# Kernel tuning notes

Hardware: AMD Instinct MI355X
Metric: run time of the kernel (lower is better)

## Reference

```python
import jax, jax.numpy as jnp
import numpy as np

N, E, H, FN, FE = 50000, 800000, 128, 8, 4


def setup_inputs() -> dict:
    key = jax.random.key(0)
    ks = jax.random.split(key, 12)
    g = lambda k, shape: jax.random.normal(k, shape, dtype=jnp.float32) * 0.05
    return dict(
        x=jax.random.normal(ks[0], (N, FN), dtype=jnp.float32),
        edge_index=jax.random.randint(ks[1], (2, E), 0, N),
        edge_attr=jax.random.normal(ks[2], (E, FE), dtype=jnp.float32),
        W1=g(ks[3], (FN, H)), b1=jnp.zeros((H,), jnp.float32),
        W2=g(ks[4], (H, H)), b2=jnp.zeros((H,), jnp.float32),
        W3=g(ks[5], (H, H)), b3=jnp.zeros((H,), jnp.float32),
        We1=g(ks[6], (FE, H)), be1=jnp.zeros((H,), jnp.float32),
        We2=g(ks[7], (H, H)), be2=jnp.zeros((H,), jnp.float32),
        Wc1=g(ks[8], (3 * H, H)), bc1=jnp.zeros((H,), jnp.float32),
        Wc2=g(ks[9], (H, H // 2)), bc2=jnp.zeros((H // 2,), jnp.float32),
        Wc3=g(ks[10], (H // 2, 2)), bc3=jnp.zeros((2,), jnp.float32),
    )


def _gcn(h, W, b, row2, col2, norm, n):
    # GCNConv: transform, normalized message from source row2 -> target col2, scatter-add, bias
    h = h @ W
    msg = norm[:, None] * h[row2]  # [E+N, H]
    return jax.ops.segment_sum(msg, col2, num_segments=n) + b


def reference(x, edge_index, edge_attr, W1, b1, W2, b2, W3, b3,
              We1, be1, We2, be2, Wc1, bc1, Wc2, bc2, Wc3, bc3):
    n = x.shape[0]
    row, col = edge_index[0], edge_index[1]
    loop = jnp.arange(n)
    # add self-loops (PyG GCNConv default)
    row2 = jnp.concatenate([row, loop])
    col2 = jnp.concatenate([col, loop])
    deg = jax.ops.segment_sum(jnp.ones_like(col2, dtype=x.dtype), col2, num_segments=n)
    dinv = jnp.where(deg > 0, deg ** -0.5, 0.0)
    norm = dinv[row2] * dinv[col2]  # symmetric normalization per edge

    h = jax.nn.relu(_gcn(x, W1, b1, row2, col2, norm, n))
    h = jax.nn.relu(_gcn(h, W2, b2, row2, col2, norm, n))
    h = jax.nn.relu(_gcn(h, W3, b3, row2, col2, norm, n))

    # edge encoder MLP (dropout inactive in eval)
    ef = jax.nn.relu(edge_attr @ We1 + be1) @ We2 + be2

    # gather endpoint node features, concat with edge features
    ec = jnp.concatenate([h[row], h[col], ef], axis=1)  # [E, 3H]
    z = jax.nn.relu(ec @ Wc1 + bc1)
    z = jax.nn.relu(z @ Wc2 + bc2)
    logits = z @ Wc3 + bc3
    return jax.nn.log_softmax(logits, axis=1)
```

## Files before the change

kernel.cpp:

```cpp
#include <hip/hip_runtime.h>
#include <math.h>

#define H 128
#define STC 152
#define SOT 136
#define SPQ 136
#define Z2S 69

typedef __attribute__((ext_vector_type(8))) short short8;
typedef __attribute__((ext_vector_type(4))) float f32x4;

__device__ inline unsigned short f2bf(float f) {
    unsigned int u = __float_as_uint(f);
    return (unsigned short)((u + 0x7fffu + ((u >> 16) & 1u)) >> 16);
}
__device__ inline float bflo(unsigned int v) { return __uint_as_float(v << 16); }
__device__ inline float bfhi(unsigned int v) { return __uint_as_float(v & 0xffff0000u); }
__device__ inline float bf2f(unsigned short v) { return __uint_as_float(((unsigned int)v) << 16); }

__device__ inline void fma4(float4& acc, float a, const float4 w) {
    acc.x = fmaf(a, w.x, acc.x);
    acc.y = fmaf(a, w.y, acc.y);
    acc.z = fmaf(a, w.z, acc.z);
    acc.w = fmaf(a, w.w, acc.w);
}


__global__ void count_kernel(const int* __restrict__ col, int E, int* __restrict__ cnt) {
    int e = blockIdx.x * blockDim.x + threadIdx.x;
    if (e < E) atomicAdd(&cnt[col[e]], 1);
}

__global__ void scan_sum_kernel(const int* __restrict__ cnt, int N, int* __restrict__ bsum) {
    int b = blockIdx.x, t = threadIdx.x;
    int base = b * 1024 + t * 4;
    int s = 0;
#pragma unroll
    for (int g = 0; g < 4; ++g) {
        int i = base + g;
        if (i < N) s += cnt[i];
    }
    for (int off = 32; off >= 1; off >>= 1) s += __shfl_down(s, off, 64);
    __shared__ int ws[4];
    if ((t & 63) == 0) ws[t >> 6] = s;
    __syncthreads();
    if (t == 0) bsum[b] = ws[0] + ws[1] + ws[2] + ws[3];
}

__global__ void scan_offsets_kernel(const int* __restrict__ bsum, int nb,
                                    int* __restrict__ boff, int* __restrict__ col_start, int N) {
    int lane = threadIdx.x;
    int v = (lane < nb) ? bsum[lane] : 0;
    int incl = v;
    for (int off = 1; off < 64; off <<= 1) {
        int u = __shfl_up(incl, off, 64);
        if (lane >= off) incl += u;
    }
    if (lane < nb) boff[lane] = incl - v;
    if (lane == 63) col_start[N] = incl;
}

__global__ void scan_write_kernel(const int* __restrict__ cnt, int N, const int* __restrict__ boff,
                                  int* __restrict__ col_start, int* __restrict__ cursor,
                                  float* __restrict__ dinv) {
    int b = blockIdx.x, t = threadIdx.x;
    int lane = t & 63, wv = t >> 6;
    int base = b * 1024 + t * 4;
    int c[4];
    int s = 0;
#pragma unroll
    for (int g = 0; g < 4; ++g) {
        int i = base + g;
        c[g] = (i < N) ? cnt[i] : 0;
        s += c[g];
    }
    int incl = s;
    for (int off = 1; off < 64; off <<= 1) {
        int u = __shfl_up(incl, off, 64);
        if (lane >= off) incl += u;
    }
    __shared__ int ws[4];
    if (lane == 63) ws[wv] = incl;
    __syncthreads();
    int run = boff[b] + incl - s;
    for (int w = 0; w < wv; ++w) run += ws[w];
#pragma unroll
    for (int g = 0; g < 4; ++g) {
        int i = base + g;
        if (i < N) {
            col_start[i] = run;
            cursor[i] = run;
            dinv[i] = rsqrtf((float)(c[g] + 1));
            run += c[g];
        }
    }
}

__global__ void scatter_kernel(const int* __restrict__ row, const int* __restrict__ col, int E,
                               int* __restrict__ cursor, int* __restrict__ csc_src,
                               int2* __restrict__ csc_ec) {
    int e = blockIdx.x * blockDim.x + threadIdx.x;
    if (e < E) {
        int c = col[e];
        int p = atomicAdd(&cursor[c], 1);
        csc_src[p] = row[e];
        csc_ec[p] = make_int2(e, c);
    }
}


__global__ __launch_bounds__(256) void aggx_kernel(
    const float* __restrict__ x, const int* __restrict__ col_start,
    const int* __restrict__ csc_src, const float* __restrict__ dinv,
    float* __restrict__ aggx, int N) {
    int wv = threadIdx.x >> 6, lane = threadIdx.x & 63;
    int i = blockIdx.x * 4 + wv;
    if (i >= N) return;
    int f = lane & 7, j = lane >> 3;
    int s0 = col_start[i], s1 = col_start[i + 1];
    float acc = 0.f;
    int p = s0 + j;
    for (; p + 8 < s1; p += 16) {
        int sa = csc_src[p], sb = csc_src[p + 8];
        float va = dinv[sa] * x[sa * 8 + f];
        float vb = dinv[sb] * x[sb * 8 + f];
        acc += va + vb;
    }
    if (p < s1) {
        int s = csc_src[p];
        acc = fmaf(dinv[s], x[s * 8 + f], acc);
    }
    acc += __shfl_xor(acc, 8, 64);
    acc += __shfl_xor(acc, 16, 64);
    acc += __shfl_xor(acc, 32, 64);
    if (j == 0) {
        float di = dinv[i];
        aggx[i * 8 + f] = fmaf(di, acc, di * di * x[i * 8 + f]);
    }
}

__global__ void xform8bf_kernel(const float* __restrict__ aggx, const float* __restrict__ W,
                                const float* __restrict__ b, const float* __restrict__ dinv,
                                unsigned int* __restrict__ out, int N) {
    int t = blockIdx.x * 256 + threadIdx.x;
    int i = t >> 6, jp = t & 63;
    if (i >= N) return;
    const float* ar = aggx + i * 8;
    float sc = dinv[i];
    int j0 = jp * 2;
    float a0 = b[j0], a1 = b[j0 + 1];
#pragma unroll
    for (int k = 0; k < 8; ++k) {
        float av = ar[k];
        a0 = fmaf(av, W[k * 128 + j0], a0);
        a1 = fmaf(av, W[k * 128 + j0 + 1], a1);
    }
    out[(size_t)i * 64 + jp] = (unsigned int)f2bf(sc * fmaxf(a0, 0.f)) |
                               ((unsigned int)f2bf(sc * fmaxf(a1, 0.f)) << 16);
}

__global__ __launch_bounds__(256) void agg128bf_kernel(
    const unsigned int* __restrict__ hd, const int* __restrict__ col_start,
    const int* __restrict__ csc_src, const float* __restrict__ dinv,
    unsigned int* __restrict__ out, int N) {
    int wv = threadIdx.x >> 6, lane = threadIdx.x & 63;
    int i = blockIdx.x * 4 + wv;
    if (i >= N) return;
    int s0 = col_start[i], s1 = col_start[i + 1];
    float ax = 0.f, ay = 0.f;
    int p = s0;
    for (; p + 16 <= s1; p += 16) {
        unsigned int v[16];
#pragma unroll
        for (int k = 0; k < 16; ++k)
            v[k] = hd[(size_t)csc_src[p + k] * 64 + lane];
#pragma unroll
        for (int k = 0; k < 16; ++k) { ax += bflo(v[k]); ay += bfhi(v[k]); }
    }
    for (; p + 4 <= s1; p += 4) {
        unsigned int v0 = hd[(size_t)csc_src[p + 0] * 64 + lane];
        unsigned int v1 = hd[(size_t)csc_src[p + 1] * 64 + lane];
        unsigned int v2 = hd[(size_t)csc_src[p + 2] * 64 + lane];
        unsigned int v3 = hd[(size_t)csc_src[p + 3] * 64 + lane];
        ax += bflo(v0) + bflo(v1) + bflo(v2) + bflo(v3);
        ay += bfhi(v0) + bfhi(v1) + bfhi(v2) + bfhi(v3);
    }
    for (; p < s1; ++p) {
        unsigned int v = hd[(size_t)csc_src[p] * 64 + lane];
        ax += bflo(v); ay += bfhi(v);
    }
    float di = dinv[i];
    unsigned int vs = hd[(size_t)i * 64 + lane];
    float rx = di * (ax + bflo(vs));
    float ry = di * (ay + bfhi(vs));
    out[(size_t)i * 64 + lane] = (unsigned int)f2bf(rx) | ((unsigned int)f2bf(ry) << 16);
}

__global__ __launch_bounds__(256) void xform_mfma_kernel(
    const unsigned short* __restrict__ in, const unsigned short* __restrict__ Bp,
    const float* __restrict__ b, const float* __restrict__ scale,
    unsigned short* __restrict__ out, int N) {
    __shared__ __align__(16) unsigned short sm[64 * STC];
    int tid = threadIdx.x;
    int i0 = blockIdx.x * 64;
    for (int u = tid; u < 1024; u += 256) {
        int i = u >> 4, l = u & 15;
        int node = i0 + i; if (node >= N) node = N - 1;
        uint4 v = ((const uint4*)in)[(size_t)node * 16 + l];
        *(uint4*)&sm[i * STC + l * 8] = v;
    }
    __syncthreads();
    int lane = tid & 63, w = tid >> 6, lm = lane & 15, quad = lane >> 4;
    int nt0 = 2 * w, nt1 = 2 * w + 1;
    f32x4 acc0[4], acc1[4];
    {
        float bv0 = b[nt0 * 16 + lm], bv1 = b[nt1 * 16 + lm];
        for (int m = 0; m < 4; ++m)
            for (int r = 0; r < 4; ++r) { acc0[m][r] = bv0; acc1[m][r] = bv1; }
    }
#pragma unroll
    for (int s = 0; s < 4; ++s) {
        short8 b0 = *(const short8*)&Bp[((size_t)(s * 8 + nt0) * 64 + lane) * 8];
        short8 b1 = *(const short8*)&Bp[((size_t)(s * 8 + nt1) * 64 + lane) * 8];
#pragma unroll
        for (int m = 0; m < 4; ++m) {
            short8 afr = *(const short8*)&sm[(m * 16 + lm) * STC + s * 32 + quad * 8];
            acc0[m] = __builtin_amdgcn_mfma_f32_16x16x32_bf16(afr, b0, acc0[m], 0, 0, 0);
            acc1[m] = __builtin_amdgcn_mfma_f32_16x16x32_bf16(afr, b1, acc1[m], 0, 0, 0);
        }
    }
    __syncthreads();
    for (int m = 0; m < 4; ++m)
        for (int r = 0; r < 4; ++r) {
            int rw = m * 16 + quad * 4 + r;
            int node = i0 + rw; if (node >= N) node = N - 1;
            float sc = scale ? scale[node] : 1.f;
            sm[rw * SOT + nt0 * 16 + lm] = f2bf(sc * fmaxf(acc0[m][r], 0.f));
            sm[rw * SOT + nt1 * 16 + lm] = f2bf(sc * fmaxf(acc1[m][r], 0.f));
        }
    __syncthreads();
    for (int u = tid; u < 1024; u += 256) {
        int i = u >> 4, l = u & 15;
        int node = i0 + i;
        if (node < N)
            *(uint4*)&out[(size_t)node * 128 + l * 8] = *(uint4*)&sm[i * SOT + l * 8];
    }
}


__global__ void weff_kernel(const float* __restrict__ We2, const float* __restrict__ Wc1,
                            float* __restrict__ Weff) {
    int idx = blockIdx.x * blockDim.x + threadIdx.x;
    int k = idx >> 7, c = idx & 127;
    float acc = 0.f;
    for (int j = 0; j < 128; ++j)
        acc = fmaf(We2[k * 128 + j], Wc1[(256 + j) * 128 + c], acc);
    Weff[idx] = acc;
}

__global__ void bc1p_kernel(const float* __restrict__ bc1, const float* __restrict__ be2,
                            const float* __restrict__ Wc1, float* __restrict__ bc1p) {
    int c = threadIdx.x;
    float acc = bc1[c];
    for (int j = 0; j < 128; ++j)
        acc = fmaf(be2[j], Wc1[(256 + j) * 128 + c], acc);
    bc1p[c] = acc;
}

__global__ void packg_kernel(const float* __restrict__ src, unsigned short* __restrict__ dst) {
    int idx = blockIdx.x * 256 + threadIdx.x;
    int s = idx >> 9, nt = (idx >> 6) & 7, lane = idx & 63;
    int quad = lane >> 4, lm = lane & 15;
    int n = nt * 16 + lm, k0 = s * 32 + quad * 8;
    unsigned int p[4];
#pragma unroll
    for (int g = 0; g < 4; ++g) {
        p[g] = (unsigned int)f2bf(src[(k0 + 2 * g) * 128 + n]) |
               ((unsigned int)f2bf(src[(k0 + 2 * g + 1) * 128 + n]) << 16);
    }
    *(uint4*)&dst[(size_t)idx * 8] = make_uint4(p[0], p[1], p[2], p[3]);
}

__global__ void pack2_kernel(const float* __restrict__ Wc2, unsigned short* __restrict__ Bp2) {
    int idx = blockIdx.x * 256 + threadIdx.x;
    int s = idx >> 8, nt = (idx >> 6) & 3, lane = idx & 63;
    int quad = lane >> 4, lm = lane & 15;
    int n = nt * 16 + lm, k0 = s * 32 + quad * 8;
    unsigned int p[4];
#pragma unroll
    for (int g = 0; g < 4; ++g) {
        p[g] = (unsigned int)f2bf(Wc2[(k0 + 2 * g) * 64 + n]) |
               ((unsigned int)f2bf(Wc2[(k0 + 2 * g + 1) * 64 + n]) << 16);
    }
    *(uint4*)&Bp2[(size_t)idx * 8] = make_uint4(p[0], p[1], p[2], p[3]);
}

__global__ void packwe1_kernel(const float* __restrict__ We1, const float* __restrict__ be1,
                               unsigned short* __restrict__ BpE) {
    int idx = blockIdx.x * 256 + threadIdx.x;
    if (idx >= 512) return;
    int nt = idx >> 6, lane = idx & 63;
    int quad = lane >> 4, lm = lane & 15;
    int n = nt * 16 + lm, k0 = quad * 8;
    unsigned int p[4];
#pragma unroll
    for (int g = 0; g < 4; ++g) {
        int r0 = k0 + 2 * g, r1 = r0 + 1;
        float v0 = (r0 < 4) ? We1[r0 * 128 + n] : ((r0 == 4) ? be1[n] : 0.f);
        float v1 = (r1 < 4) ? We1[r1 * 128 + n] : ((r1 == 4) ? be1[n] : 0.f);
        p[g] = (unsigned int)f2bf(v0) | ((unsigned int)f2bf(v1) << 16);
    }
    *(uint4*)&BpE[(size_t)idx * 8] = make_uint4(p[0], p[1], p[2], p[3]);
}


__global__ __launch_bounds__(256) void h3pq_kernel(
    const unsigned short* __restrict__ in, const unsigned short* __restrict__ BpW3,
    const float* __restrict__ b3,
    const unsigned short* __restrict__ BpA, const unsigned short* __restrict__ BpB,
    const float* __restrict__ bc1p,
    unsigned short* __restrict__ P, unsigned short* __restrict__ Q, int N) {
    __shared__ __align__(16) unsigned short At[64 * STC];
    __shared__ __align__(16) unsigned short Hs[64 * SOT];
    int tid = threadIdx.x;
    int i0 = blockIdx.x * 64;
    for (int u = tid; u < 1024; u += 256) {
        int i = u >> 4, l = u & 15;
        int node = i0 + i; if (node >= N) node = N - 1;
        uint4 v = ((const uint4*)in)[(size_t)node * 16 + l];
        *(uint4*)&At[i * STC + l * 8] = v;
    }
    __syncthreads();
    int lane = tid & 63, w = tid >> 6, lm = lane & 15, quad = lane >> 4;

    {
        int nt0 = 2 * w, nt1 = 2 * w + 1;
        f32x4 a0[4], a1[4];
        float bv0 = b3[nt0 * 16 + lm], bv1 = b3[nt1 * 16 + lm];
        for (int m = 0; m < 4; ++m)
            for (int r = 0; r < 4; ++r) { a0[m][r] = bv0; a1[m][r] = bv1; }
#pragma unroll
        for (int s = 0; s < 4; ++s) {
            short8 b0 = *(const short8*)&BpW3[((size_t)(s * 8 + nt0) * 64 + lane) * 8];
            short8 b1 = *(const short8*)&BpW3[((size_t)(s * 8 + nt1) * 64 + lane) * 8];
#pragma unroll
            for (int m = 0; m < 4; ++m) {
                short8 afr = *(const short8*)&At[(m * 16 + lm) * STC + s * 32 + quad * 8];
                a0[m] = __builtin_amdgcn_mfma_f32_16x16x32_bf16(afr, b0, a0[m], 0, 0, 0);
                a1[m] = __builtin_amdgcn_mfma_f32_16x16x32_bf16(afr, b1, a1[m], 0, 0, 0);
            }
        }
        __syncthreads();
        for (int m = 0; m < 4; ++m)
            for (int r = 0; r < 4; ++r) {
                int rw = m * 16 + quad * 4 + r;
                Hs[rw * SOT + nt0 * 16 + lm] = f2bf(fmaxf(a0[m][r], 0.f));
                Hs[rw * SOT + nt1 * 16 + lm] = f2bf(fmaxf(a1[m][r], 0.f));
            }
    }
    __syncthreads();

    int half = w & 1;
    const unsigned short* Bp = (w >> 1) ? BpB : BpA;
    f32x4 acc[4][4];
    for (int nt = 0; nt < 4; ++nt) {
        float bv = (w >> 1) ? 0.f : bc1p[half * 64 + nt * 16 + lm];
        for (int m = 0; m < 4; ++m)
            for (int r = 0; r < 4; ++r) acc[nt][m][r] = bv;
    }
#pragma unroll
    for (int s = 0; s < 4; ++s) {
        short8 afr[4];
#pragma unroll
        for (int m = 0; m < 4; ++m)
            afr[m] = *(const short8*)&Hs[(m * 16 + lm) * SOT + s * 32 + quad * 8];
#pragma unroll
        for (int nt = 0; nt < 4; ++nt) {
            short8 bfr = *(const short8*)&Bp[((size_t)(s * 8 + half * 4 + nt) * 64 + lane) * 8];
#pragma unroll
            for (int m = 0; m < 4; ++m)
                acc[nt][m] = __builtin_amdgcn_mfma_f32_16x16x32_bf16(afr[m], bfr, acc[nt][m], 0, 0, 0);
        }
    }
    __syncthreads();
    unsigned short* St = At;

    if (w < 2) {
        for (int nt = 0; nt < 4; ++nt)
            for (int m = 0; m < 4; ++m)
                for (int r = 0; r < 4; ++r) {
                    int rw = m * 16 + quad * 4 + r;
                    St[rw * SOT + half * 64 + nt * 16 + lm] = f2bf(acc[nt][m][r]);
                }
    }
    __syncthreads();
    for (int u = tid; u < 1024; u += 256) {
        int i = u >> 4, l = u & 15;
        int node = i0 + i;
        if (node < N)
            *(uint4*)&P[(size_t)node * 128 + l * 8] = *(uint4*)&St[i * SOT + l * 8];
    }
    __syncthreads();
    if (w >= 2) {
        for (int nt = 0; nt < 4; ++nt)
            for (int m = 0; m < 4; ++m)
                for (int r = 0; r < 4; ++r) {
                    int rw = m * 16 + quad * 4 + r;
                    St[rw * SOT + half * 64 + nt * 16 + lm] = f2bf(acc[nt][m][r]);
                }
    }
    __syncthreads();
    for (int u = tid; u < 1024; u += 256) {
        int i = u >> 4, l = u & 15;
        int node = i0 + i;
        if (node < N)
            *(uint4*)&Q[(size_t)node * 128 + l * 8] = *(uint4*)&St[i * SOT + l * 8];
    }
}


__global__ __launch_bounds__(256, 4) void classifier_mfma2(
    const int* __restrict__ csc_src, const int2* __restrict__ csc_ec,
    const float* __restrict__ ea, const unsigned short* __restrict__ BpE,
    const unsigned short* __restrict__ P, const unsigned short* __restrict__ Q,
    const unsigned short* __restrict__ BpU, const unsigned short* __restrict__ Bp2,
    const float* __restrict__ bc2, const float* __restrict__ Wc3, const float* __restrict__ bc3,
    float* __restrict__ out, int E) {
    __shared__ __align__(16) unsigned char smem[37888];
    unsigned short* SpqB = (unsigned short*)smem;
    float* z2 = (float*)smem;
    unsigned short* At = (unsigned short*)(smem + 17664);
    unsigned short* z1 = At;
    float* part = (float*)(smem + 17664);
    int* sS = (int*)(smem + 37120);
    int* eS = sS + 64;
    int* cS = eS + 64;

    int tid = threadIdx.x;
    int lane = tid & 63, w = tid >> 6, lm = lane & 15, quad = lane >> 4;
    int e0 = blockIdx.x * 64;

    short8 bE0 = *(const short8*)&BpE[((size_t)(2 * w) * 64 + lane) * 8];
    short8 bE1 = *(const short8*)&BpE[((size_t)(2 * w + 1) * 64 + lane) * 8];
    short8 b0s[4], b1s[4], b2s[4];
#pragma unroll
    for (int s = 0; s < 4; ++s) {
        b0s[s] = *(const short8*)&BpU[((size_t)(s * 8 + 2 * w) * 64 + lane) * 8];
        b1s[s] = *(const short8*)&BpU[((size_t)(s * 8 + 2 * w + 1) * 64 + lane) * 8];
        b2s[s] = *(const short8*)&Bp2[((size_t)(s * 4 + w) * 64 + lane) * 8];
    }
    float bv2 = bc2[w * 16 + lm];

    if (tid < 64) {
        int p = e0 + tid; if (p >= E) p = E - 1;
        sS[tid] = csc_src[p];
        int2 ec = csc_ec[p];
        eS[tid] = ec.x; cS[tid] = ec.y;
    }
    __syncthreads();

    {
        const uint4* P4 = (const uint4*)P;
        const uint4* Q4 = (const uint4*)Q;
        int l = tid & 15;
#pragma unroll
        for (int j = 0; j < 4; ++j) {
            int i = (tid >> 4) + 16 * j;
            uint4 pv = P4[(size_t)sS[i] * 16 + l];
            uint4 qv = Q4[(size_t)cS[i] * 16 + l];
            unsigned int o0 = (unsigned int)f2bf(bflo(pv.x) + bflo(qv.x)) |
                              ((unsigned int)f2bf(bfhi(pv.x) + bfhi(qv.x)) << 16);
            unsigned int o1 = (unsigned int)f2bf(bflo(pv.y) + bflo(qv.y)) |
                              ((unsigned int)f2bf(bfhi(pv.y) + bfhi(qv.y)) << 16);
            unsigned int o2 = (unsigned int)f2bf(bflo(pv.z) + bflo(qv.z)) |
                              ((unsigned int)f2bf(bfhi(pv.z) + bfhi(qv.z)) << 16);
            unsigned int o3 = (unsigned int)f2bf(bflo(pv.w) + bflo(qv.w)) |
                              ((unsigned int)f2bf(bfhi(pv.w) + bfhi(qv.w)) << 16);
            *(uint4*)&SpqB[i * SPQ + l * 8] = make_uint4(o0, o1, o2, o3);
        }
    }

    short8 eaf[4];
#pragma unroll
    for (int m = 0; m < 4; ++m) eaf[m] = (short8){0, 0, 0, 0, 0, 0, 0, 0};
    if (quad == 0) {
#pragma unroll
        for (int m = 0; m < 4; ++m) {
            int ed = eS[m * 16 + lm];
            float4 a = ((const float4*)ea)[ed];
            eaf[m][0] = (short)f2bf(a.x);
            eaf[m][1] = (short)f2bf(a.y);
            eaf[m][2] = (short)f2bf(a.z);
            eaf[m][3] = (short)f2bf(a.w);
            eaf[m][4] = (short)0x3F80;
        }
    }

    {
        f32x4 zacc = {0.f, 0.f, 0.f, 0.f};
#pragma unroll
        for (int m = 0; m < 4; ++m) {
            f32x4 t0 = __builtin_amdgcn_mfma_f32_16x16x32_bf16(eaf[m], bE0, zacc, 0, 0, 0);
            f32x4 t1 = __builtin_amdgcn_mfma_f32_16x16x32_bf16(eaf[m], bE1, zacc, 0, 0, 0);
#pragma unroll
            for (int r = 0; r < 4; ++r) {
                int rw = m * 16 + quad * 4 + r;
                At[rw * STC + 32 * w + lm]      = f2bf(fmaxf(t0[r], 0.f));
                At[rw * STC + 32 * w + 16 + lm] = f2bf(fmaxf(t1[r], 0.f));
            }
        }
    }
    __syncthreads();

    f32x4 acc0[4], acc1[4];
    for (int m = 0; m < 4; ++m)
        for (int r = 0; r < 4; ++r) { acc0[m][r] = 0.f; acc1[m][r] = 0.f; }
#pragma unroll
    for (int s = 0; s < 4; ++s) {
#pragma unroll
        for (int m = 0; m < 4; ++m) {
            short8 afr = *(const short8*)&At[(m * 16 + lm) * STC + s * 32 + quad * 8];
            acc0[m] = __builtin_amdgcn_mfma_f32_16x16x32_bf16(afr, b0s[s], acc0[m], 0, 0, 0);
            acc1[m] = __builtin_amdgcn_mfma_f32_16x16x32_bf16(afr, b1s[s], acc1[m], 0, 0, 0);
        }
    }
    for (int m = 0; m < 4; ++m)
        for (int r = 0; r < 4; ++r) {
            int rw = m * 16 + quad * 4 + r;
            acc0[m][r] = fmaxf(acc0[m][r] + bf2f(SpqB[rw * SPQ + 32 * w + lm]), 0.f);
            acc1[m][r] = fmaxf(acc1[m][r] + bf2f(SpqB[rw * SPQ + 32 * w + 16 + lm]), 0.f);
        }
    __syncthreads();
    for (int m = 0; m < 4; ++m)
        for (int r = 0; r < 4; ++r) {
            int rw = m * 16 + quad * 4 + r;
            z1[rw * STC + 32 * w + lm]      = f2bf(acc0[m][r]);
            z1[rw * STC + 32 * w + 16 + lm] = f2bf(acc1[m][r]);
        }
    __syncthreads();

    {
        f32x4 acc2[4];
        for (int m = 0; m < 4; ++m)
            for (int r = 0; r < 4; ++r) acc2[m][r] = bv2;
#pragma unroll
        for (int s = 0; s < 4; ++s) {
#pragma unroll
            for (int m = 0; m < 4; ++m) {
                short8 afr = *(const short8*)&z1[(m * 16 + lm) * STC + s * 32 + quad * 8];
                acc2[m] = __builtin_amdgcn_mfma_f32_16x16x32_bf16(afr, b2s[s], acc2[m], 0, 0, 0);
            }
        }
        for (int m = 0; m < 4; ++m)
            for (int r = 0; r < 4; ++r)
                z2[(m * 16 + quad * 4 + r) * Z2S + w * 16 + lm] = fmaxf(acc2[m][r], 0.f);
    }
    __syncthreads();

    {
        int e = tid & 63, q = tid >> 6;
        int c = q & 1, hf = q >> 1;
        const float* zr = z2 + e * Z2S + hf * 32;
        const float* wc = Wc3 + hf * 64 + c;
        float acc = 0.f;
#pragma unroll 8
        for (int kk = 0; kk < 32; ++kk)
            acc = fmaf(zr[kk], wc[2 * kk], acc);
        part[q * 64 + e] = acc;
    }
    __syncthreads();
    if (tid < 64) {
        int p = e0 + tid;
        if (p < E) {
            float l0 = bc3[0] + part[tid] + part[128 + tid];
            float l1 = bc3[1] + part[64 + tid] + part[192 + tid];
            float m = fmaxf(l0, l1);
            float lse = m + logf(expf(l0 - m) + expf(l1 - m));
            ((float2*)out)[eS[tid]] = make_float2(l0 - lse, l1 - lse);
        }
    }
}


extern "C" void kernel_launch(void* const* d_in, const int* in_sizes, int n_in,
                              void* d_out, int out_size, void* d_ws, size_t ws_size,
                              hipStream_t stream) {
    const float* x   = (const float*)d_in[0];
    const int*   ei  = (const int*)d_in[1];
    const float* ea  = (const float*)d_in[2];
    const float* W1  = (const float*)d_in[3];
    const float* b1  = (const float*)d_in[4];
    const float* W2  = (const float*)d_in[5];
    const float* b2  = (const float*)d_in[6];
    const float* W3  = (const float*)d_in[7];
    const float* b3  = (const float*)d_in[8];
    const float* We1 = (const float*)d_in[9];
    const float* be1 = (const float*)d_in[10];
    const float* We2 = (const float*)d_in[11];
    const float* be2 = (const float*)d_in[12];
    const float* Wc1 = (const float*)d_in[13];
    const float* bc1 = (const float*)d_in[14];
    const float* Wc2 = (const float*)d_in[15];
    const float* bc2 = (const float*)d_in[16];
    const float* Wc3 = (const float*)d_in[17];
    const float* bc3 = (const float*)d_in[18];
    float* out = (float*)d_out;

    int N = in_sizes[0] / 8;
    int E = in_sizes[1] / 2;
    const int* row = ei;
    const int* col = ei + E;
    int NB = (N + 1023) / 1024;
    int ntiles = (E + 63) / 64;

    char* w = (char*)d_ws;
    auto alloc = [&](size_t bytes) { void* p = (void*)w; w += (bytes + 255) & ~(size_t)255; return p; };
    int*   cnt       = (int*)alloc((size_t)N * 4);
    int*   col_start = (int*)alloc((size_t)(N + 1) * 4);
    int*   cursor    = (int*)alloc((size_t)N * 4);
    int*   csc_src   = (int*)alloc((size_t)E * 4);
    int2*  csc_ec    = (int2*)alloc((size_t)E * 8);
    float* dinv      = (float*)alloc((size_t)N * 4);
    int*   bsum      = (int*)alloc(64 * 4);
    int*   boff      = (int*)alloc(64 * 4);
    float* Weff      = (float*)alloc(128 * 128 * 4);
    float* bc1p      = (float*)alloc(128 * 4);
    unsigned short* BpA  = (unsigned short*)alloc(32768);
    unsigned short* BpB  = (unsigned short*)alloc(32768);
    unsigned short* BpU  = (unsigned short*)alloc(32768);
    unsigned short* BpW2 = (unsigned short*)alloc(32768);
    unsigned short* BpW3 = (unsigned short*)alloc(32768);
    unsigned short* Bp2  = (unsigned short*)alloc(16384);
    unsigned short* BpE  = (unsigned short*)alloc(8192);
    float* aggx = (float*)alloc((size_t)N * 8 * 4);
    unsigned short* bufA = (unsigned short*)alloc((size_t)N * H * 2);
    unsigned short* bufB = (unsigned short*)alloc((size_t)N * H * 2);
    unsigned short* Pm   = (unsigned short*)alloc((size_t)N * H * 2);
    unsigned short* Qm   = (unsigned short*)alloc((size_t)N * H * 2);

    hipMemsetAsync(cnt, 0, (size_t)N * 4, stream);
    count_kernel<<<(E + 255) / 256, 256, 0, stream>>>(col, E, cnt);
    scan_sum_kernel<<<NB, 256, 0, stream>>>(cnt, N, bsum);
    scan_offsets_kernel<<<1, 64, 0, stream>>>(bsum, NB, boff, col_start, N);
    scan_write_kernel<<<NB, 256, 0, stream>>>(cnt, N, boff, col_start, cursor, dinv);
    scatter_kernel<<<(E + 255) / 256, 256, 0, stream>>>(row, col, E, cursor, csc_src, csc_ec);

    weff_kernel<<<64, 256, 0, stream>>>(We2, Wc1, Weff);
    bc1p_kernel<<<1, 128, 0, stream>>>(bc1, be2, Wc1, bc1p);
    packg_kernel<<<8, 256, 0, stream>>>(Wc1, BpA);
    packg_kernel<<<8, 256, 0, stream>>>(Wc1 + 128 * 128, BpB);
    packg_kernel<<<8, 256, 0, stream>>>(Weff, BpU);
    packg_kernel<<<8, 256, 0, stream>>>(W2, BpW2);
    packg_kernel<<<8, 256, 0, stream>>>(W3, BpW3);
    pack2_kernel<<<4, 256, 0, stream>>>(Wc2, Bp2);
    packwe1_kernel<<<2, 256, 0, stream>>>(We1, be1, BpE);

    aggx_kernel<<<(N + 3) / 4, 256, 0, stream>>>(x, col_start, csc_src, dinv, aggx, N);
    xform8bf_kernel<<<(N * 64 + 255) / 256, 256, 0, stream>>>(aggx, W1, b1, dinv,
                                                              (unsigned int*)bufA, N);
    agg128bf_kernel<<<(N + 3) / 4, 256, 0, stream>>>((const unsigned int*)bufA, col_start, csc_src,
                                                     dinv, (unsigned int*)bufB, N);
    xform_mfma_kernel<<<(N + 63) / 64, 256, 0, stream>>>(bufB, BpW2, b2, dinv, bufA, N);
    agg128bf_kernel<<<(N + 3) / 4, 256, 0, stream>>>((const unsigned int*)bufA, col_start, csc_src,
                                                     dinv, (unsigned int*)bufB, N);
    h3pq_kernel<<<(N + 63) / 64, 256, 0, stream>>>(bufB, BpW3, b3, BpA, BpB, bc1p, Pm, Qm, N);

    classifier_mfma2<<<ntiles, 256, 0, stream>>>(
        csc_src, csc_ec, ea, BpE, Pm, Qm, BpU, Bp2, bc2, Wc3, bc3, out, E);
}
```

Baseline: 461.7 us.

## Process four edge tiles per classifier block with P-row prefetch and hardware bf16 packing

The classifier kernel now handles four 64-edge tiles per block. It loads all edge indices at once and prefetches the next tile's P rows into registers while the current tile's MFMA work runs, amortizing per-block weight-fragment loads and hiding gather latency. Separately, the software round-to-nearest float-to-bf16 conversion is replaced everywhere with the v_cvt_pk_bf16_f32 instruction, which packs two values per op. The cost is fewer blocks (less parallelism and tail balance), extra registers for the prefetch, and slightly more shared memory.

Result: slower. 604.2 us (+30.9%).

```diff
diff --git a/kernel.cpp b/kernel.cpp
--- a/kernel.cpp
+++ b/kernel.cpp
@@ -10,19 +10,19 @@
 typedef __attribute__((ext_vector_type(8))) short short8;
 typedef __attribute__((ext_vector_type(4))) float f32x4;
 
-__device__ inline unsigned short f2bf(float f) {
-    unsigned int u = __float_as_uint(f);
-    return (unsigned short)((u + 0x7fffu + ((u >> 16) & 1u)) >> 16);
-}
 __device__ inline float bflo(unsigned int v) { return __uint_as_float(v << 16); }
 __device__ inline float bfhi(unsigned int v) { return __uint_as_float(v & 0xffff0000u); }
 __device__ inline float bf2f(unsigned short v) { return __uint_as_float(((unsigned int)v) << 16); }
 
-__device__ inline void fma4(float4& acc, float a, const float4 w) {
-    acc.x = fmaf(a, w.x, acc.x);
-    acc.y = fmaf(a, w.y, acc.y);
-    acc.z = fmaf(a, w.z, acc.z);
-    acc.w = fmaf(a, w.w, acc.w);
+__device__ inline unsigned int cvtpk(float lo, float hi) {
+    unsigned int r;
+    asm("v_cvt_pk_bf16_f32 %0, %1, %2" : "=v"(r) : "v"(lo), "v"(hi));
+    return r;
+}
+__device__ inline unsigned short f2bf1(float f) {
+    unsigned int r;
+    asm("v_cvt_pk_bf16_f32 %0, %1, %1" : "=v"(r) : "v"(f));
+    return (unsigned short)r;
 }
 
 
@@ -155,8 +155,7 @@
         a0 = fmaf(av, W[k * 128 + j0], a0);
         a1 = fmaf(av, W[k * 128 + j0 + 1], a1);
     }
-    out[(size_t)i * 64 + jp] = (unsigned int)f2bf(sc * fmaxf(a0, 0.f)) |
-                               ((unsigned int)f2bf(sc * fmaxf(a1, 0.f)) << 16);
+    out[(size_t)i * 64 + jp] = cvtpk(sc * fmaxf(a0, 0.f), sc * fmaxf(a1, 0.f));
 }
 
 __global__ __launch_bounds__(256) void agg128bf_kernel(
@@ -193,7 +192,7 @@
     unsigned int vs = hd[(size_t)i * 64 + lane];
     float rx = di * (ax + bflo(vs));
     float ry = di * (ay + bfhi(vs));
-    out[(size_t)i * 64 + lane] = (unsigned int)f2bf(rx) | ((unsigned int)f2bf(ry) << 16);
+    out[(size_t)i * 64 + lane] = cvtpk(rx, ry);
 }
 
 __global__ __launch_bounds__(256) void xform_mfma_kernel(
@@ -235,8 +234,8 @@
             int rw = m * 16 + quad * 4 + r;
             int node = i0 + rw; if (node >= N) node = N - 1;
             float sc = scale ? scale[node] : 1.f;
-            sm[rw * SOT + nt0 * 16 + lm] = f2bf(sc * fmaxf(acc0[m][r], 0.f));
-            sm[rw * SOT + nt1 * 16 + lm] = f2bf(sc * fmaxf(acc1[m][r], 0.f));
+            sm[rw * SOT + nt0 * 16 + lm] = f2bf1(sc * fmaxf(acc0[m][r], 0.f));
+            sm[rw * SOT + nt1 * 16 + lm] = f2bf1(sc * fmaxf(acc1[m][r], 0.f));
         }
     __syncthreads();
     for (int u = tid; u < 1024; u += 256) {
@@ -274,10 +273,8 @@
     int n = nt * 16 + lm, k0 = s * 32 + quad * 8;
     unsigned int p[4];
 #pragma unroll
-    for (int g = 0; g < 4; ++g) {
-        p[g] = (unsigned int)f2bf(src[(k0 + 2 * g) * 128 + n]) |
-               ((unsigned int)f2bf(src[(k0 + 2 * g + 1) * 128 + n]) << 16);
-    }
+    for (int g = 0; g < 4; ++g)
+        p[g] = cvtpk(src[(k0 + 2 * g) * 128 + n], src[(k0 + 2 * g + 1) * 128 + n]);
     *(uint4*)&dst[(size_t)idx * 8] = make_uint4(p[0], p[1], p[2], p[3]);
 }
 
@@ -288,10 +285,8 @@
     int n = nt * 16 + lm, k0 = s * 32 + quad * 8;
     unsigned int p[4];
 #pragma unroll
-    for (int g = 0; g < 4; ++g) {
-        p[g] = (unsigned int)f2bf(Wc2[(k0 + 2 * g) * 64 + n]) |
-               ((unsigned int)f2bf(Wc2[(k0 + 2 * g + 1) * 64 + n]) << 16);
-    }
+    for (int g = 0; g < 4; ++g)
+        p[g] = cvtpk(Wc2[(k0 + 2 * g) * 64 + n], Wc2[(k0 + 2 * g + 1) * 64 + n]);
     *(uint4*)&Bp2[(size_t)idx * 8] = make_uint4(p[0], p[1], p[2], p[3]);
 }
 
@@ -308,7 +303,7 @@
         int r0 = k0 + 2 * g, r1 = r0 + 1;
         float v0 = (r0 < 4) ? We1[r0 * 128 + n] : ((r0 == 4) ? be1[n] : 0.f);
         float v1 = (r1 < 4) ? We1[r1 * 128 + n] : ((r1 == 4) ? be1[n] : 0.f);
-        p[g] = (unsigned int)f2bf(v0) | ((unsigned int)f2bf(v1) << 16);
+        p[g] = cvtpk(v0, v1);
     }
     *(uint4*)&BpE[(size_t)idx * 8] = make_uint4(p[0], p[1], p[2], p[3]);
 }
@@ -354,8 +349,8 @@
         for (int m = 0; m < 4; ++m)
             for (int r = 0; r < 4; ++r) {
                 int rw = m * 16 + quad * 4 + r;
-                Hs[rw * SOT + nt0 * 16 + lm] = f2bf(fmaxf(a0[m][r], 0.f));
-                Hs[rw * SOT + nt1 * 16 + lm] = f2bf(fmaxf(a1[m][r], 0.f));
+                Hs[rw * SOT + nt0 * 16 + lm] = f2bf1(fmaxf(a0[m][r], 0.f));
+                Hs[rw * SOT + nt1 * 16 + lm] = f2bf1(fmaxf(a1[m][r], 0.f));
             }
     }
     __syncthreads();
@@ -390,7 +385,7 @@
             for (int m = 0; m < 4; ++m)
                 for (int r = 0; r < 4; ++r) {
                     int rw = m * 16 + quad * 4 + r;
-                    St[rw * SOT + half * 64 + nt * 16 + lm] = f2bf(acc[nt][m][r]);
+                    St[rw * SOT + half * 64 + nt * 16 + lm] = f2bf1(acc[nt][m][r]);
                 }
     }
     __syncthreads();
@@ -406,7 +401,7 @@
             for (int m = 0; m < 4; ++m)
                 for (int r = 0; r < 4; ++r) {
                     int rw = m * 16 + quad * 4 + r;
-                    St[rw * SOT + half * 64 + nt * 16 + lm] = f2bf(acc[nt][m][r]);
+                    St[rw * SOT + half * 64 + nt * 16 + lm] = f2bf1(acc[nt][m][r]);
                 }
     }
     __syncthreads();
@@ -418,6 +413,8 @@
     }
 }
 
+
+#define CTILES 4
 
 __global__ __launch_bounds__(256, 4) void classifier_mfma2(
     const int* __restrict__ csc_src, const int2* __restrict__ csc_ec,
@@ -426,19 +423,19 @@
     const unsigned short* __restrict__ BpU, const unsigned short* __restrict__ Bp2,
     const float* __restrict__ bc2, const float* __restrict__ Wc3, const float* __restrict__ bc3,
     float* __restrict__ out, int E) {
-    __shared__ __align__(16) unsigned char smem[37888];
+    __shared__ __align__(16) unsigned char smem[40192];
     unsigned short* SpqB = (unsigned short*)smem;
     float* z2 = (float*)smem;
     unsigned short* At = (unsigned short*)(smem + 17664);
     unsigned short* z1 = At;
     float* part = (float*)(smem + 17664);
     int* sS = (int*)(smem + 37120);
-    int* eS = sS + 64;
-    int* cS = eS + 64;
+    int* eS = sS + 64 * CTILES;
+    int* cS = eS + 64 * CTILES;
 
     int tid = threadIdx.x;
     int lane = tid & 63, w = tid >> 6, lm = lane & 15, quad = lane >> 4;
-    int e0 = blockIdx.x * 64;
+    int base = blockIdx.x * (64 * CTILES);
 
     short8 bE0 = *(const short8*)&BpE[((size_t)(2 * w) * 64 + lane) * 8];
     short8 bE1 = *(const short8*)&BpE[((size_t)(2 * w + 1) * 64 + lane) * 8];
@@ -451,133 +448,148 @@
     }
     float bv2 = bc2[w * 16 + lm];
 
-    if (tid < 64) {
-        int p = e0 + tid; if (p >= E) p = E - 1;
+    {
+        int p = base + tid; if (p >= E) p = E - 1;
         sS[tid] = csc_src[p];
         int2 ec = csc_ec[p];
         eS[tid] = ec.x; cS[tid] = ec.y;
     }
     __syncthreads();
 
-    {
-        const uint4* P4 = (const uint4*)P;
-        const uint4* Q4 = (const uint4*)Q;
-        int l = tid & 15;
+    const uint4* P4 = (const uint4*)P;
+    const uint4* Q4 = (const uint4*)Q;
+    int rbase = tid >> 4;
+
+    uint4 pv[4];
+#pragma unroll
+    for (int j = 0; j < 4; ++j)
+        pv[j] = P4[(size_t)sS[rbase + 16 * j] * 16 + lm];
+
+#pragma unroll
+    for (int t = 0; t < CTILES; ++t) {
+        int e0 = base + t * 64;
+        if (e0 >= E) break;
+        const int* eSc = eS + t * 64;
+        const int* cSc = cS + t * 64;
+
 #pragma unroll
         for (int j = 0; j < 4; ++j) {
-            int i = (tid >> 4) + 16 * j;
-            uint4 pv = P4[(size_t)sS[i] * 16 + l];
-            uint4 qv = Q4[(size_t)cS[i] * 16 + l];
-            unsigned int o0 = (unsigned int)f2bf(bflo(pv.x) + bflo(qv.x)) |
-                              ((unsigned int)f2bf(bfhi(pv.x) + bfhi(qv.x)) << 16);
-            unsigned int o1 = (unsigned int)f2bf(bflo(pv.y) + bflo(qv.y)) |
-                              ((unsigned int)f2bf(bfhi(pv.y) + bfhi(qv.y)) << 16);
-            unsigned int o2 = (unsigned int)f2bf(bflo(pv.z) + bflo(qv.z)) |
-                              ((unsigned int)f2bf(bfhi(pv.z) + bfhi(qv.z)) << 16);
-            unsigned int o3 = (unsigned int)f2bf(bflo(pv.w) + bflo(qv.w)) |
-                              ((unsigned int)f2bf(bfhi(pv.w) + bfhi(qv.w)) << 16);
-            *(uint4*)&SpqB[i * SPQ + l * 8] = make_uint4(o0, o1, o2, o3);
-        }
-    }
-
-    short8 eaf[4];
-#pragma unroll
-    for (int m = 0; m < 4; ++m) eaf[m] = (short8){0, 0, 0, 0, 0, 0, 0, 0};
-    if (quad == 0) {
-#pragma unroll
-        for (int m = 0; m < 4; ++m) {
-            int ed = eS[m * 16 + lm];
-            float4 a = ((const float4*)ea)[ed];
-            eaf[m][0] = (short)f2bf(a.x);
-            eaf[m][1] = (short)f2bf(a.y);
-            eaf[m][2] = (short)f2bf(a.z);
-            eaf[m][3] = (short)f2bf(a.w);
-            eaf[m][4] = (short)0x3F80;
-        }
-    }
-
-    {
-        f32x4 zacc = {0.f, 0.f, 0.f, 0.f};
-#pragma unroll
-        for (int m = 0; m < 4; ++m) {
-            f32x4 t0 = __builtin_amdgcn_mfma_f32_16x16x32_bf16(eaf[m], bE0, zacc, 0, 0, 0);
-            f32x4 t1 = __builtin_amdgcn_mfma_f32_16x16x32_bf16(eaf[m], bE1, zacc, 0, 0, 0);
-#pragma unroll
+            int i = rbase + 16 * j;
+            uint4 qv = Q4[(size_t)cSc[i] * 16 + lm];
+            uint4 o;
+            o.x = cvtpk(bflo(pv[j].x) + bflo(qv.x), bfhi(pv[j].x) + bfhi(qv.x));
+            o.y = cvtpk(bflo(pv[j].y) + bflo(qv.y), bfhi(pv[j].y) + bfhi(qv.y));
+            o.z = cvtpk(bflo(pv[j].z) + bflo(qv.z), bfhi(pv[j].z) + bfhi(qv.z));
+            o.w = cvtpk(bflo(pv[j].w) + bflo(qv.w), bfhi(pv[j].w) + bfhi(qv.w));
+            *(uint4*)&SpqB[i * SPQ + lm * 8] = o;
+        }
+
+        short8 eaf[4];
+#pragma unroll
+        for (int m = 0; m < 4; ++m) eaf[m] = (short8){0, 0, 0, 0, 0, 0, 0, 0};
+        if (quad == 0) {
+#pragma unroll
+            for (int m = 0; m < 4; ++m) {
+                int ed = eSc[m * 16 + lm];
+                float4 a = ((const float4*)ea)[ed];
+                eaf[m][0] = (short)f2bf1(a.x);
+                eaf[m][1] = (short)f2bf1(a.y);
+                eaf[m][2] = (short)f2bf1(a.z);
+                eaf[m][3] = (short)f2bf1(a.w);
+                eaf[m][4] = (short)0x3F80;
+            }
+        }
+
+        {
+            f32x4 zacc = {0.f, 0.f, 0.f, 0.f};
+#pragma unroll
+            for (int m = 0; m < 4; ++m) {
+                f32x4 t0 = __builtin_amdgcn_mfma_f32_16x16x32_bf16(eaf[m], bE0, zacc, 0, 0, 0);
+                f32x4 t1 = __builtin_amdgcn_mfma_f32_16x16x32_bf16(eaf[m], bE1, zacc, 0, 0, 0);
+#pragma unroll
+                for (int r = 0; r < 4; ++r) {
+                    int rw = m * 16 + quad * 4 + r;
+                    At[rw * STC + 32 * w + lm]      = f2bf1(fmaxf(t0[r], 0.f));
+                    At[rw * STC + 32 * w + 16 + lm] = f2bf1(fmaxf(t1[r], 0.f));
+                }
+            }
+        }
+        __syncthreads();
+
+        if (t + 1 < CTILES && base + (t + 1) * 64 < E) {
+#pragma unroll
+            for (int j = 0; j < 4; ++j)
+                pv[j] = P4[(size_t)sS[(t + 1) * 64 + rbase + 16 * j] * 16 + lm];
+        }
+
+        f32x4 acc0[4], acc1[4];
+        for (int m = 0; m < 4; ++m)
+            for (int r = 0; r < 4; ++r) { acc0[m][r] = 0.f; acc1[m][r] = 0.f; }
+#pragma unroll
+        for (int s = 0; s < 4; ++s) {
+#pragma unroll
+            for (int m = 0; m < 4; ++m) {
+                short8 afr = *(const short8*)&At[(m * 16 + lm) * STC + s * 32 + quad * 8];
+                acc0[m] = __builtin_amdgcn_mfma_f32_16x16x32_bf16(afr, b0s[s], acc0[m], 0, 0, 0);
+                acc1[m] = __builtin_amdgcn_mfma_f32_16x16x32_bf16(afr, b1s[s], acc1[m], 0, 0, 0);
+            }
+        }
+        for (int m = 0; m < 4; ++m)
             for (int r = 0; r < 4; ++r) {
                 int rw = m * 16 + quad * 4 + r;
-                At[rw * STC + 32 * w + lm]      = f2bf(fmaxf(t0[r], 0.f));
-                At[rw * STC + 32 * w + 16 + lm] = f2bf(fmaxf(t1[r], 0.f));
-            }
-        }
-    }
-    __syncthreads();
-
-    f32x4 acc0[4], acc1[4];
-    for (int m = 0; m < 4; ++m)
-        for (int r = 0; r < 4; ++r) { acc0[m][r] = 0.f; acc1[m][r] = 0.f; }
-#pragma unroll
-    for (int s = 0; s < 4; ++s) {
-#pragma unroll
-        for (int m = 0; m < 4; ++m) {
-            short8 afr = *(const short8*)&At[(m * 16 + lm) * STC + s * 32 + quad * 8];
-            acc0[m] = __builtin_amdgcn_mfma_f32_16x16x32_bf16(afr, b0s[s], acc0[m], 0, 0, 0);
-            acc1[m] = __builtin_amdgcn_mfma_f32_16x16x32_bf16(afr, b1s[s], acc1[m], 0, 0, 0);
-        }
-    }
-    for (int m = 0; m < 4; ++m)
-        for (int r = 0; r < 4; ++r) {
-            int rw = m * 16 + quad * 4 + r;
-            acc0[m][r] = fmaxf(acc0[m][r] + bf2f(SpqB[rw * SPQ + 32 * w + lm]), 0.f);
-            acc1[m][r] = fmaxf(acc1[m][r] + bf2f(SpqB[rw * SPQ + 32 * w + 16 + lm]), 0.f);
-        }
-    __syncthreads();
-    for (int m = 0; m < 4; ++m)
-        for (int r = 0; r < 4; ++r) {
-            int rw = m * 16 + quad * 4 + r;
-            z1[rw * STC + 32 * w + lm]      = f2bf(acc0[m][r]);
-            z1[rw * STC + 32 * w + 16 + lm] = f2bf(acc1[m][r]);
-        }
-    __syncthreads();
-
-    {
-        f32x4 acc2[4];
-        for (int m = 0; m < 4; ++m)
-            for (int r = 0; r < 4; ++r) acc2[m][r] = bv2;
-#pragma unroll
-        for (int s = 0; s < 4; ++s) {
-#pragma unroll
-            for (int m = 0; m < 4; ++m) {
-                short8 afr = *(const short8*)&z1[(m * 16 + lm) * STC + s * 32 + quad * 8];
-                acc2[m] = __builtin_amdgcn_mfma_f32_16x16x32_bf16(afr, b2s[s], acc2[m], 0, 0, 0);
-            }
-        }
-        for (int m = 0; m < 4; ++m)
-            for (int r = 0; r < 4; ++r)
-                z2[(m * 16 + quad * 4 + r) * Z2S + w * 16 + lm] = fmaxf(acc2[m][r], 0.f);
-    }
-    __syncthreads();
-
-    {
-        int e = tid & 63, q = tid >> 6;
-        int c = q & 1, hf = q >> 1;
-        const float* zr = z2 + e * Z2S + hf * 32;
-        const float* wc = Wc3 + hf * 64 + c;
-        float acc = 0.f;
+                acc0[m][r] = fmaxf(acc0[m][r] + bf2f(SpqB[rw * SPQ + 32 * w + lm]), 0.f);
+                acc1[m][r] = fmaxf(acc1[m][r] + bf2f(SpqB[rw * SPQ + 32 * w + 16 + lm]), 0.f);
+            }
+        __syncthreads();
+        for (int m = 0; m < 4; ++m)
+            for (int r = 0; r < 4; ++r) {
+                int rw = m * 16 + quad * 4 + r;
+                z1[rw * STC + 32 * w + lm]      = f2bf1(acc0[m][r]);
+                z1[rw * STC + 32 * w + 16 + lm] = f2bf1(acc1[m][r]);
+            }
+        __syncthreads();
+
+        {
+            f32x4 acc2[4];
+            for (int m = 0; m < 4; ++m)
+                for (int r = 0; r < 4; ++r) acc2[m][r] = bv2;
+#pragma unroll
+            for (int s = 0; s < 4; ++s) {
+#pragma unroll
+                for (int m = 0; m < 4; ++m) {
+                    short8 afr = *(const short8*)&z1[(m * 16 + lm) * STC + s * 32 + quad * 8];
+                    acc2[m] = __builtin_amdgcn_mfma_f32_16x16x32_bf16(afr, b2s[s], acc2[m], 0, 0, 0);
+                }
+            }
+            for (int m = 0; m < 4; ++m)
+                for (int r = 0; r < 4; ++r)
+                    z2[(m * 16 + quad * 4 + r) * Z2S + w * 16 + lm] = fmaxf(acc2[m][r], 0.f);
+        }
+        __syncthreads();
+
+        {
+            int e = tid & 63, q = tid >> 6;
+            int c = q & 1, hf = q >> 1;
+            const float* zr = z2 + e * Z2S + hf * 32;
+            const float* wc = Wc3 + hf * 64 + c;
+            float acc = 0.f;
 #pragma unroll 8
-        for (int kk = 0; kk < 32; ++kk)
-            acc = fmaf(zr[kk], wc[2 * kk], acc);
-        part[q * 64 + e] = acc;
-    }
-    __syncthreads();
-    if (tid < 64) {
-        int p = e0 + tid;
-        if (p < E) {
-            float l0 = bc3[0] + part[tid] + part[128 + tid];
-            float l1 = bc3[1] + part[64 + tid] + part[192 + tid];
-            float m = fmaxf(l0, l1);
-            float lse = m + logf(expf(l0 - m) + expf(l1 - m));
-            ((float2*)out)[eS[tid]] = make_float2(l0 - lse, l1 - lse);
-        }
+            for (int kk = 0; kk < 32; ++kk)
+                acc = fmaf(zr[kk], wc[2 * kk], acc);
+            part[q * 64 + e] = acc;
+        }
+        __syncthreads();
+        if (tid < 64) {
+            int p = e0 + tid;
+            if (p < E) {
+                float l0 = bc3[0] + part[tid] + part[128 + tid];
+                float l1 = bc3[1] + part[64 + tid] + part[192 + tid];
+                float m = fmaxf(l0, l1);
+                float lse = m + logf(expf(l0 - m) + expf(l1 - m));
+                ((float2*)out)[eSc[tid]] = make_float2(l0 - lse, l1 - lse);
+            }
+        }
+        __syncthreads();
     }
 }
 
@@ -611,7 +623,7 @@
     const int* row = ei;
     const int* col = ei + E;
     int NB = (N + 1023) / 1024;
-    int ntiles = (E + 63) / 64;
+    int nblk_cls = (E + 64 * CTILES - 1) / (64 * CTILES);
 
     char* w = (char*)d_ws;
     auto alloc = [&](size_t bytes) { void* p = (void*)w; w += (bytes + 255) & ~(size_t)255; return p; };
@@ -665,6 +677,6 @@
                                                      dinv, (unsigned int*)bufB, N);
     h3pq_kernel<<<(N + 63) / 64, 256, 0, stream>>>(bufB, BpW3, b3, BpA, BpB, bc1p, Pm, Qm, N);
 
-    classifier_mfma2<<<ntiles, 256, 0, stream>>>(
+    classifier_mfma2<<<nblk_cls, 256, 0, stream>>>(
         csc_src, csc_ec, ea, BpE, Pm, Qm, BpU, Bp2, bc2, Wc3, bc3, out, E);
 }
```
